# Optimization experiments

Hardware: AMD Instinct MI355X
Metric: run time of the kernel (lower is better)

The kernel has to match this reference:

```python
import jax, jax.numpy as jnp
import numpy as np

N, E, T = 10000, 160000, 1600000
D, C, H = 256, 64, 1024  # d_model, d_message/channels, 4*d_model ffn hidden


def setup_inputs() -> dict:
    key = jax.random.key(0)
    ks = jax.random.split(key, 20)
    rn = lambda k, s, sc=1.0: jax.random.normal(k, s, dtype=jnp.float32) * sc
    return {
        "x": rn(ks[0], (N, D)),
        "y": rn(ks[1], (E, D)),
        "r": rn(ks[2], (E, 3)),
        "src": jax.random.randint(ks[3], (E,), 0, N),
        "dst": jax.random.randint(ks[4], (E,), 0, N),
        "tsrc": jax.random.randint(ks[5], (T,), 0, E),
        "tdst": jax.random.randint(ks[6], (T,), 0, E),
        "W_src": rn(ks[7], (D, C), 0.05), "b_src": rn(ks[8], (C,), 0.05),
        "W_dst": rn(ks[9], (D, C), 0.05), "b_dst": rn(ks[10], (C,), 0.05),
        "W_edge": rn(ks[11], (D, C), 0.05), "b_edge": rn(ks[12], (C,), 0.05),
        "attn": rn(ks[13], (C,), 0.05),
        "W1": rn(ks[14], (C, H), 0.05), "b1": rn(ks[15], (H,), 0.05),
        "W2": rn(ks[16], (H, D), 0.05), "b2": rn(ks[17], (D,), 0.05),
    }


def reference(x, y, r, src, dst, tsrc, tdst,
              W_src, b_src, W_dst, b_dst, W_edge, b_edge,
              attn, W1, b1, W2, b2):
    # per-bond message: xij = Lin_src(x)[src] + Lin_dst(x)[dst] + Lin_edge(y)  -> (E, C)
    xij = (x @ W_src + b_src)[src] + (x @ W_dst + b_dst)[dst] + (y @ W_edge + b_edge)

    # triplet angle cosine via normalized (negated) bond vectors  -> (T,)
    rnorm = -r / jnp.linalg.norm(r, axis=1, keepdims=True)
    cos_jik = jnp.clip(jnp.sum(rnorm[tsrc] * rnorm[tdst], axis=-1), -1.0 + 1e-6, 1.0 - 1e-6)

    # Chebyshev expansion: T_n(cos) = cos(n * arccos(cos))  -> (T, C)
    n = jnp.arange(C, dtype=jnp.float32)
    z_jik = jnp.cos(n[None, :] * jnp.arccos(cos_jik)[:, None])

    # triplet feature and attention logit
    e_jik = jax.nn.silu(z_jik + xij[tsrc] + xij[tdst])          # (T, C)
    logits = e_jik @ attn                                        # (T,)

    # segment softmax over triplets grouped by destination bond (edge_softmax)
    mx = jax.ops.segment_max(logits, tdst, num_segments=E)
    ex = jnp.exp(logits - mx[tdst])
    den = jax.ops.segment_sum(ex, tdst, num_segments=E)
    a = ex / den[tdst]                                           # (T,)

    # attention-weighted scatter-sum of neighbor bond features  -> (E, C)
    ft = jax.ops.segment_sum(xij[tsrc] * a[:, None], tdst, num_segments=E)

    # feedforward: Linear -> SiLU -> Linear  -> (E, D)
    return jax.nn.silu(ft @ W1 + b1) @ W2 + b2
```

## Files before the change

kernel.cpp:

```cpp
#include <hip/hip_runtime.h>

#define N_NODES 10000
#define N_EDGES 160000
#define N_TRI   1600000
#define DM      256
#define CH      64
#define HH      1024

typedef short bf16x8 __attribute__((ext_vector_type(8)));
typedef float f32x4  __attribute__((ext_vector_type(4)));

__device__ __forceinline__ unsigned short f2bf(float f) {
  unsigned int u = __float_as_uint(f);
  u += 0x7fff + ((u >> 16) & 1);
  return (unsigned short)(u >> 16);
}

__global__ __launch_bounds__(256) void k_node_proj(
    const float* __restrict__ x, const float* __restrict__ Ws, const float* __restrict__ bs,
    const float* __restrict__ Wd, const float* __restrict__ bd,
    float* __restrict__ xs, float* __restrict__ xd) {
  __shared__ float xl[4][DM];
  int tid = threadIdx.x;
  int n0 = blockIdx.x * 4;
  for (int i = tid; i < 4 * DM; i += 256) xl[i >> 8][i & 255] = x[n0 * DM + i];
  __syncthreads();
  int c = tid & 63, g = tid >> 6;
  float as = bs[c], ad = bd[c];
  for (int d = 0; d < DM; d++) {
    float xv = xl[g][d];
    as += xv * Ws[d * CH + c];
    ad += xv * Wd[d * CH + c];
  }
  int n = n0 + g;
  xs[n * CH + c] = as;
  xd[n * CH + c] = ad;
}

__global__ __launch_bounds__(256) void k_edge_proj(
    const float* __restrict__ y, const float* __restrict__ We, const float* __restrict__ be,
    const float* __restrict__ xs, const float* __restrict__ xd,
    const int* __restrict__ src, const int* __restrict__ dst,
    float* __restrict__ xij) {
  __shared__ float yl[16][DM];
  int tid = threadIdx.x;
  int e0 = blockIdx.x * 16;
  for (int i = tid; i < 16 * DM; i += 256) yl[i >> 8][i & 255] = y[e0 * DM + i];
  __syncthreads();
  int c = tid & 63, g = tid >> 6;
  float acc[4];
#pragma unroll
  for (int s = 0; s < 4; s++) acc[s] = be[c];
  for (int d = 0; d < DM; d += 4) {
    float w0 = We[(d + 0) * CH + c];
    float w1 = We[(d + 1) * CH + c];
    float w2 = We[(d + 2) * CH + c];
    float w3 = We[(d + 3) * CH + c];
#pragma unroll
    for (int s = 0; s < 4; s++) {
      const float4 yv = *(const float4*)&yl[g * 4 + s][d];
      acc[s] += yv.x * w0 + yv.y * w1 + yv.z * w2 + yv.w * w3;
    }
  }
#pragma unroll
  for (int s = 0; s < 4; s++) {
    int e = e0 + g * 4 + s;
    xij[e * CH + c] = acc[s] + xs[src[e] * CH + c] + xd[dst[e] * CH + c];
  }
}

__global__ void k_rnorm(const float* __restrict__ r, float4* __restrict__ rn4) {
  int e = blockIdx.x * 256 + threadIdx.x;
  if (e >= N_EDGES) return;
  float a = r[e * 3 + 0], b = r[e * 3 + 1], c = r[e * 3 + 2];
  float inv = rsqrtf(a * a + b * b + c * c);
  rn4[e] = (float4){-a * inv, -b * inv, -c * inv, 0.f};
}

__global__ __launch_bounds__(256) void k_theta(
    const float4* __restrict__ rn4, const int* __restrict__ tsrc, const int* __restrict__ tdst,
    float* __restrict__ theta) {
  int t = blockIdx.x * 256 + threadIdx.x;
  if (t >= N_TRI) return;
  float4 a = rn4[tsrc[t]];
  float4 b = rn4[tdst[t]];
  float c = a.x * b.x + a.y * b.y + a.z * b.z;
  c = fminf(fmaxf(c, -1.0f + 1e-6f), 1.0f - 1e-6f);
  theta[t] = acosf(c);
}

__global__ void k_hist(const int* __restrict__ tdst, int* __restrict__ cnt) {
  int t = blockIdx.x * 256 + threadIdx.x;
  if (t < N_TRI) atomicAdd(&cnt[tdst[t]], 1);
}

__global__ __launch_bounds__(256) void k_scan_sum(const int* __restrict__ cnt,
                                                  int* __restrict__ bsum, int n) {
  __shared__ int s[256];
  int b = blockIdx.x, tid = threadIdx.x;
  int tot = 0;
#pragma unroll
  for (int i = 0; i < 8; i++) {
    int idx = b * 2048 + i * 256 + tid;
    if (idx < n) tot += cnt[idx];
  }
  s[tid] = tot;
  __syncthreads();
  for (int off = 128; off > 0; off >>= 1) {
    if (tid < off) s[tid] += s[tid + off];
    __syncthreads();
  }
  if (tid == 0) bsum[b] = s[0];
}

__global__ void k_scan_top(int* __restrict__ bsum, int nb, int* __restrict__ start_last) {
  if (threadIdx.x == 0) {
    int run = 0;
    for (int i = 0; i < nb; i++) {
      int v = bsum[i];
      bsum[i] = run;
      run += v;
    }
    *start_last = run;
  }
}

__global__ __launch_bounds__(256) void k_scan_apply(const int* __restrict__ cnt,
                                                    const int* __restrict__ bsum,
                                                    int* __restrict__ start,
                                                    int* __restrict__ cur, int n) {
  __shared__ int s[256];
  int b = blockIdx.x, tid = threadIdx.x;
  int base = b * 2048 + tid * 8;
  int loc[8];
  int tot = 0;
#pragma unroll
  for (int i = 0; i < 8; i++) {
    int idx = base + i;
    int v = (idx < n) ? cnt[idx] : 0;
    loc[i] = tot;
    tot += v;
  }
  s[tid] = tot;
  __syncthreads();
  for (int off = 1; off < 256; off <<= 1) {
    int t2 = 0;
    if (tid >= off) t2 = s[tid - off];
    __syncthreads();
    if (tid >= off) s[tid] += t2;
    __syncthreads();
  }
  int excl = s[tid] - tot + bsum[b];
#pragma unroll
  for (int i = 0; i < 8; i++) {
    int idx = base + i;
    if (idx < n) {
      int v = excl + loc[i];
      start[idx] = v;
      cur[idx] = v;
    }
  }
}

__global__ void k_scatter(const int* __restrict__ tdst, int* __restrict__ cur,
                          int* __restrict__ sorted) {
  int t = blockIdx.x * 256 + threadIdx.x;
  if (t < N_TRI) {
    int p = atomicAdd(&cur[tdst[t]], 1);
    sorted[p] = t;
  }
}

__global__ __launch_bounds__(256) void k_attn_ft(
    const int* __restrict__ start, const int* __restrict__ sorted,
    const float* __restrict__ theta, const int* __restrict__ tsrc,
    const float* __restrict__ xij, const float* __restrict__ attn,
    unsigned short* __restrict__ ft) {
  int tid = threadIdx.x;
  int e = blockIdx.x * 4 + (tid >> 6);
  int lane = tid & 63;
  float lanef = (float)lane;
  int beg = start[e], end = start[e + 1];
  int deg = end - beg;
  float xd = xij[e * CH + lane];
  float av = attn[lane];
  float m = -1e30f, den = 0.f, acc = 0.f;
  if (deg > 0 && deg <= 64) {
    int ts_ = 0;
    float th_ = 0.f;
    if (lane < deg) {
      int t = sorted[beg + lane];
      ts_ = tsrc[t];
      th_ = theta[t];
    }
    int ts_cur = __shfl(ts_, 0);
    float th_cur = __shfl(th_, 0);
    float xs_cur = xij[ts_cur * CH + lane];
    for (int i = 0; i < deg; i++) {
      float th_nxt = 0.f, xs_nxt = 0.f;
      if (i + 1 < deg) {
        int ts_nxt = __shfl(ts_, i + 1);
        th_nxt = __shfl(th_, i + 1);
        xs_nxt = xij[ts_nxt * CH + lane];
      }
      float v = __cosf(th_cur * lanef) + xs_cur + xd;
      float sv = v / (1.f + __expf(-v));
      float contrib = sv * av;
#pragma unroll
      for (int off = 32; off; off >>= 1) contrib += __shfl_xor(contrib, off);
      float mn = fmaxf(m, contrib);
      float scale = __expf(m - mn);
      float p = __expf(contrib - mn);
      den = den * scale + p;
      acc = acc * scale + p * xs_cur;
      m = mn;
      th_cur = th_nxt;
      xs_cur = xs_nxt;
    }
  } else if (deg > 64) {
    for (int i = 0; i < deg; i++) {
      int t = sorted[beg + i];
      int ts = tsrc[t];
      float th = theta[t];
      float xs = xij[ts * CH + lane];
      float v = __cosf(th * lanef) + xs + xd;
      float sv = v / (1.f + __expf(-v));
      float contrib = sv * av;
#pragma unroll
      for (int off = 32; off; off >>= 1) contrib += __shfl_xor(contrib, off);
      float mn = fmaxf(m, contrib);
      float scale = __expf(m - mn);
      float p = __expf(contrib - mn);
      den = den * scale + p;
      acc = acc * scale + p * xs;
      m = mn;
    }
  }
  ft[e * CH + lane] = f2bf(deg > 0 ? acc / den : 0.f);
}

__global__ __launch_bounds__(256) void k_prep_w1p(const float* __restrict__ W1,
                                                  unsigned short* __restrict__ W1P) {
  int idx = blockIdx.x * 256 + threadIdx.x;
  int k = idx & 63, row = idx >> 6;
  int i = row & 15, t = (row >> 4) & 1, hb = row >> 5;
  int hidden = hb * 32 + ((i >> 2) << 3) + (t << 2) + (i & 3);
  W1P[idx] = f2bf(W1[k * HH + hidden]);
}

__global__ __launch_bounds__(256) void k_prep_w2t(const float* __restrict__ W2,
                                                  unsigned short* __restrict__ W2T) {
  int idx = blockIdx.x * 256 + threadIdx.x;
  int n = idx >> 10, k = idx & 1023;
  W2T[idx] = f2bf(W2[k * DM + n]);
}

__global__ __launch_bounds__(256, 2) void k_ffn_mfma2(
    const unsigned short* __restrict__ ft, const unsigned short* __restrict__ W1P,
    const float* __restrict__ b1, const unsigned short* __restrict__ W2T,
    const float* __restrict__ b2, float* __restrict__ out) {
  int tid = threadIdx.x;
  int wave = tid >> 6, lane = tid & 63;
  int l16 = lane & 15, q = lane >> 4;
  int ebase = blockIdx.x * 128 + wave * 32;

  bf16x8 ftf[2][2];
#pragma unroll
  for (int mt = 0; mt < 2; mt++)
#pragma unroll
    for (int s = 0; s < 2; s++)
      ftf[mt][s] = *(const bf16x8*)&ft[(size_t)(ebase + mt * 16 + l16) * CH + s * 32 + q * 8];

  f32x4 acc[2][16];
#pragma unroll
  for (int mt = 0; mt < 2; mt++)
#pragma unroll
    for (int nt = 0; nt < 16; nt++) acc[mt][nt] = (f32x4){0.f, 0.f, 0.f, 0.f};

  bf16x8 w1f[2][2];
#pragma unroll
  for (int t = 0; t < 2; t++)
#pragma unroll
    for (int s = 0; s < 2; s++)
      w1f[t][s] = *(const bf16x8*)&W1P[(size_t)((t * 16) + l16) * 64 + s * 32 + q * 8];

  for (int hb = 0; hb < 32; hb++) {
    f32x4 h[2][2];
#pragma unroll
    for (int mt = 0; mt < 2; mt++)
#pragma unroll
      for (int t = 0; t < 2; t++) {
        f32x4 z = (f32x4){0.f, 0.f, 0.f, 0.f};
        z = __builtin_amdgcn_mfma_f32_16x16x32_bf16(w1f[t][0], ftf[mt][0], z, 0, 0, 0);
        z = __builtin_amdgcn_mfma_f32_16x16x32_bf16(w1f[t][1], ftf[mt][1], z, 0, 0, 0);
        h[mt][t] = z;
      }

    int hbn = (hb < 31) ? hb + 1 : 31;
    bf16x8 w1n[2][2];
#pragma unroll
    for (int t = 0; t < 2; t++)
#pragma unroll
      for (int s = 0; s < 2; s++)
        w1n[t][s] = *(const bf16x8*)&W1P[(size_t)((hbn * 2 + t) * 16 + l16) * 64 + s * 32 + q * 8];

    const float4 b1v0 = *(const float4*)&b1[hb * 32 + q * 8];
    const float4 b1v1 = *(const float4*)&b1[hb * 32 + q * 8 + 4];
    union { bf16x8 v; unsigned int u[4]; } pa[2];
#pragma unroll
    for (int mt = 0; mt < 2; mt++) {
      float v0 = h[mt][0][0] + b1v0.x, v1 = h[mt][0][1] + b1v0.y;
      float v2 = h[mt][0][2] + b1v0.z, v3 = h[mt][0][3] + b1v0.w;
      float w0 = h[mt][1][0] + b1v1.x, w1 = h[mt][1][1] + b1v1.y;
      float w2 = h[mt][1][2] + b1v1.z, w3 = h[mt][1][3] + b1v1.w;
      float s0 = v0 / (1.f + __expf(-v0)), s1 = v1 / (1.f + __expf(-v1));
      float s2 = v2 / (1.f + __expf(-v2)), s3 = v3 / (1.f + __expf(-v3));
      float t0 = w0 / (1.f + __expf(-w0)), t1 = w1 / (1.f + __expf(-w1));
      float t2 = w2 / (1.f + __expf(-w2)), t3 = w3 / (1.f + __expf(-w3));
      pa[mt].u[0] = ((unsigned int)f2bf(s1) << 16) | f2bf(s0);
      pa[mt].u[1] = ((unsigned int)f2bf(s3) << 16) | f2bf(s2);
      pa[mt].u[2] = ((unsigned int)f2bf(t1) << 16) | f2bf(t0);
      pa[mt].u[3] = ((unsigned int)f2bf(t3) << 16) | f2bf(t2);
    }

#pragma unroll
    for (int ng = 0; ng < 4; ng++) {
      bf16x8 bw[4];
#pragma unroll
      for (int i = 0; i < 4; i++)
        bw[i] = *(const bf16x8*)&W2T[(size_t)((ng * 4 + i) * 16 + l16) * HH + hb * 32 + q * 8];
#pragma unroll
      for (int i = 0; i < 4; i++) {
        acc[0][ng * 4 + i] =
            __builtin_amdgcn_mfma_f32_16x16x32_bf16(pa[0].v, bw[i], acc[0][ng * 4 + i], 0, 0, 0);
        acc[1][ng * 4 + i] =
            __builtin_amdgcn_mfma_f32_16x16x32_bf16(pa[1].v, bw[i], acc[1][ng * 4 + i], 0, 0, 0);
      }
    }

#pragma unroll
    for (int t = 0; t < 2; t++)
#pragma unroll
      for (int s = 0; s < 2; s++) w1f[t][s] = w1n[t][s];
  }

#pragma unroll
  for (int nt = 0; nt < 16; nt++) {
    float b2v = b2[nt * 16 + l16];
#pragma unroll
    for (int mt = 0; mt < 2; mt++) {
      int erow = ebase + mt * 16 + q * 4;
#pragma unroll
      for (int r = 0; r < 4; r++)
        out[(size_t)(erow + r) * DM + nt * 16 + l16] = acc[mt][nt][r] + b2v;
    }
  }
}

extern "C" void kernel_launch(void* const* d_in, const int* in_sizes, int n_in,
                              void* d_out, int out_size, void* d_ws, size_t ws_size,
                              hipStream_t stream) {
  (void)in_sizes; (void)n_in; (void)out_size; (void)ws_size;
  const float* x      = (const float*)d_in[0];
  const float* y      = (const float*)d_in[1];
  const float* r      = (const float*)d_in[2];
  const int*   src    = (const int*)d_in[3];
  const int*   dst    = (const int*)d_in[4];
  const int*   tsrc   = (const int*)d_in[5];
  const int*   tdst   = (const int*)d_in[6];
  const float* W_src  = (const float*)d_in[7];
  const float* b_src  = (const float*)d_in[8];
  const float* W_dst  = (const float*)d_in[9];
  const float* b_dst  = (const float*)d_in[10];
  const float* W_edge = (const float*)d_in[11];
  const float* b_edge = (const float*)d_in[12];
  const float* attn   = (const float*)d_in[13];
  const float* W1     = (const float*)d_in[14];
  const float* b1     = (const float*)d_in[15];
  const float* W2     = (const float*)d_in[16];
  const float* b2     = (const float*)d_in[17];
  float* out = (float*)d_out;

  char* wsp = (char*)d_ws;
  auto alloc = [&](size_t bytes) -> char* {
    char* p = wsp;
    wsp += (bytes + 255) & ~(size_t)255;
    return p;
  };
  float* xs     = (float*)alloc((size_t)N_NODES * CH * 4);
  float* xd     = (float*)alloc((size_t)N_NODES * CH * 4);
  float* xij    = (float*)alloc((size_t)N_EDGES * CH * 4);
  float4* rn4   = (float4*)alloc((size_t)N_EDGES * 16);
  float* theta  = (float*)alloc((size_t)N_TRI * 4);
  int*   cnt    = (int*)alloc((size_t)N_EDGES * 4);
  int*   start  = (int*)alloc((size_t)(N_EDGES + 1) * 4);
  int*   cur    = (int*)alloc((size_t)N_EDGES * 4);
  int*   bsum   = (int*)alloc(1024 * 4);
  int*   sorted = (int*)alloc((size_t)N_TRI * 4);
  unsigned short* ftb = (unsigned short*)alloc((size_t)N_EDGES * CH * 2);
  unsigned short* W1P = (unsigned short*)alloc((size_t)CH * HH * 2);
  unsigned short* W2T = (unsigned short*)alloc((size_t)HH * DM * 2);

  const int NB = (N_EDGES + 2047) / 2048;

  k_prep_w1p<<<(CH * HH) / 256, 256, 0, stream>>>(W1, W1P);
  k_prep_w2t<<<(HH * DM) / 256, 256, 0, stream>>>(W2, W2T);

  k_node_proj<<<N_NODES / 4, 256, 0, stream>>>(x, W_src, b_src, W_dst, b_dst, xs, xd);
  k_rnorm<<<N_EDGES / 256, 256, 0, stream>>>(r, rn4);
  k_edge_proj<<<N_EDGES / 16, 256, 0, stream>>>(y, W_edge, b_edge, xs, xd, src, dst, xij);
  k_theta<<<N_TRI / 256, 256, 0, stream>>>(rn4, tsrc, tdst, theta);

  hipMemsetAsync(cnt, 0, (size_t)N_EDGES * 4, stream);
  k_hist<<<N_TRI / 256, 256, 0, stream>>>(tdst, cnt);
  k_scan_sum<<<NB, 256, 0, stream>>>(cnt, bsum, N_EDGES);
  k_scan_top<<<1, 64, 0, stream>>>(bsum, NB, &start[N_EDGES]);
  k_scan_apply<<<NB, 256, 0, stream>>>(cnt, bsum, start, cur, N_EDGES);
  k_scatter<<<N_TRI / 256, 256, 0, stream>>>(tdst, cur, sorted);

  k_attn_ft<<<N_EDGES / 4, 256, 0, stream>>>(start, sorted, theta, tsrc, xij, attn, ftb);
  k_ffn_mfma2<<<N_EDGES / 128, 256, 0, stream>>>(ftb, W1P, b1, W2T, b2, out);
}
```

Measured before the change: 1.318 ms.

## Split FFN output columns across waves and share hidden activations via LDS

The FFN kernel now gives each block 64 edges, and each wave computes the hidden activations for its own 16 edges. Those activations go through a double-buffered shared-memory tile, so each wave can then produce a 64-column slice of the output for all 64 edges. This cuts accumulator registers from 32 to 16 tiles per wave and raises the occupancy target from 2 to 3 blocks. The costs are a __syncthreads per hidden block, extra LDS traffic, and twice as many blocks, each reading its own W2 slice.

```diff
diff --git a/kernel.cpp b/kernel.cpp
--- a/kernel.cpp
+++ b/kernel.cpp
@@ -255,46 +255,62 @@
   W2T[idx] = f2bf(W2[k * DM + n]);
 }
 
-__global__ __launch_bounds__(256, 2) void k_ffn_mfma2(
+__global__ __launch_bounds__(256, 3) void k_ffn_mfma3(
     const unsigned short* __restrict__ ft, const unsigned short* __restrict__ W1P,
     const float* __restrict__ b1, const unsigned short* __restrict__ W2T,
     const float* __restrict__ b2, float* __restrict__ out) {
+  __shared__ __align__(16) unsigned short hbuf[2][4 * 64 * 8];
   int tid = threadIdx.x;
-  int wave = tid >> 6, lane = tid & 63;
+  int w = tid >> 6, lane = tid & 63;
   int l16 = lane & 15, q = lane >> 4;
-  int ebase = blockIdx.x * 128 + wave * 32;
-
-  bf16x8 ftf[2][2];
-#pragma unroll
-  for (int mt = 0; mt < 2; mt++)
+  int e0 = blockIdx.x * 64;
+
+  bf16x8 ftf[2];
+#pragma unroll
+  for (int s = 0; s < 2; s++)
+    ftf[s] = *(const bf16x8*)&ft[(size_t)(e0 + w * 16 + l16) * CH + s * 32 + q * 8];
+
+  f32x4 acc[4][4];
+#pragma unroll
+  for (int mt = 0; mt < 4; mt++)
+#pragma unroll
+    for (int nt = 0; nt < 4; nt++) acc[mt][nt] = (f32x4){0.f, 0.f, 0.f, 0.f};
+
+  bf16x8 w1f[2][2];
+#pragma unroll
+  for (int t = 0; t < 2; t++)
 #pragma unroll
     for (int s = 0; s < 2; s++)
-      ftf[mt][s] = *(const bf16x8*)&ft[(size_t)(ebase + mt * 16 + l16) * CH + s * 32 + q * 8];
-
-  f32x4 acc[2][16];
-#pragma unroll
-  for (int mt = 0; mt < 2; mt++)
-#pragma unroll
-    for (int nt = 0; nt < 16; nt++) acc[mt][nt] = (f32x4){0.f, 0.f, 0.f, 0.f};
-
-  bf16x8 w1f[2][2];
-#pragma unroll
-  for (int t = 0; t < 2; t++)
-#pragma unroll
-    for (int s = 0; s < 2; s++)
-      w1f[t][s] = *(const bf16x8*)&W1P[(size_t)((t * 16) + l16) * 64 + s * 32 + q * 8];
-
+      w1f[t][s] = *(const bf16x8*)&W1P[(size_t)(t * 16 + l16) * 64 + s * 32 + q * 8];
+
+  int p = 0;
   for (int hb = 0; hb < 32; hb++) {
-    f32x4 h[2][2];
-#pragma unroll
-    for (int mt = 0; mt < 2; mt++)
-#pragma unroll
-      for (int t = 0; t < 2; t++) {
-        f32x4 z = (f32x4){0.f, 0.f, 0.f, 0.f};
-        z = __builtin_amdgcn_mfma_f32_16x16x32_bf16(w1f[t][0], ftf[mt][0], z, 0, 0, 0);
-        z = __builtin_amdgcn_mfma_f32_16x16x32_bf16(w1f[t][1], ftf[mt][1], z, 0, 0, 0);
-        h[mt][t] = z;
-      }
+    bf16x8 bw[4];
+#pragma unroll
+    for (int nt = 0; nt < 4; nt++)
+      bw[nt] = *(const bf16x8*)&W2T[(size_t)(w * 64 + nt * 16 + l16) * HH + hb * 32 + q * 8];
+
+    f32x4 h0 = (f32x4){0.f, 0.f, 0.f, 0.f};
+    f32x4 h1 = (f32x4){0.f, 0.f, 0.f, 0.f};
+    h0 = __builtin_amdgcn_mfma_f32_16x16x32_bf16(w1f[0][0], ftf[0], h0, 0, 0, 0);
+    h0 = __builtin_amdgcn_mfma_f32_16x16x32_bf16(w1f[0][1], ftf[1], h0, 0, 0, 0);
+    h1 = __builtin_amdgcn_mfma_f32_16x16x32_bf16(w1f[1][0], ftf[0], h1, 0, 0, 0);
+    h1 = __builtin_amdgcn_mfma_f32_16x16x32_bf16(w1f[1][1], ftf[1], h1, 0, 0, 0);
+
+    const float4 bv0 = *(const float4*)&b1[hb * 32 + q * 8];
+    const float4 bv1 = *(const float4*)&b1[hb * 32 + q * 8 + 4];
+    float v0 = h0[0] + bv0.x, v1 = h0[1] + bv0.y, v2 = h0[2] + bv0.z, v3 = h0[3] + bv0.w;
+    float w0 = h1[0] + bv1.x, w1_ = h1[1] + bv1.y, w2 = h1[2] + bv1.z, w3 = h1[3] + bv1.w;
+    float s0 = v0 / (1.f + __expf(-v0)), s1 = v1 / (1.f + __expf(-v1));
+    float s2 = v2 / (1.f + __expf(-v2)), s3 = v3 / (1.f + __expf(-v3));
+    float t0 = w0 / (1.f + __expf(-w0)), t1 = w1_ / (1.f + __expf(-w1_));
+    float t2 = w2 / (1.f + __expf(-w2)), t3 = w3 / (1.f + __expf(-w3));
+    union { bf16x8 v; unsigned int u[4]; } pa;
+    pa.u[0] = ((unsigned int)f2bf(s1) << 16) | f2bf(s0);
+    pa.u[1] = ((unsigned int)f2bf(s3) << 16) | f2bf(s2);
+    pa.u[2] = ((unsigned int)f2bf(t1) << 16) | f2bf(t0);
+    pa.u[3] = ((unsigned int)f2bf(t3) << 16) | f2bf(t2);
+    *(bf16x8*)&hbuf[p][(w * 64 + lane) * 8] = pa.v;
 
     int hbn = (hb < 31) ? hb + 1 : 31;
     bf16x8 w1n[2][2];
@@ -304,55 +320,35 @@
       for (int s = 0; s < 2; s++)
         w1n[t][s] = *(const bf16x8*)&W1P[(size_t)((hbn * 2 + t) * 16 + l16) * 64 + s * 32 + q * 8];
 
-    const float4 b1v0 = *(const float4*)&b1[hb * 32 + q * 8];
-    const float4 b1v1 = *(const float4*)&b1[hb * 32 + q * 8 + 4];
-    union { bf16x8 v; unsigned int u[4]; } pa[2];
-#pragma unroll
-    for (int mt = 0; mt < 2; mt++) {
-      float v0 = h[mt][0][0] + b1v0.x, v1 = h[mt][0][1] + b1v0.y;
-      float v2 = h[mt][0][2] + b1v0.z, v3 = h[mt][0][3] + b1v0.w;
-      float w0 = h[mt][1][0] + b1v1.x, w1 = h[mt][1][1] + b1v1.y;
-      float w2 = h[mt][1][2] + b1v1.z, w3 = h[mt][1][3] + b1v1.w;
-      float s0 = v0 / (1.f + __expf(-v0)), s1 = v1 / (1.f + __expf(-v1));
-      float s2 = v2 / (1.f + __expf(-v2)), s3 = v3 / (1.f + __expf(-v3));
-      float t0 = w0 / (1.f + __expf(-w0)), t1 = w1 / (1.f + __expf(-w1));
-      float t2 = w2 / (1.f + __expf(-w2)), t3 = w3 / (1.f + __expf(-w3));
-      pa[mt].u[0] = ((unsigned int)f2bf(s1) << 16) | f2bf(s0);
-      pa[mt].u[1] = ((unsigned int)f2bf(s3) << 16) | f2bf(s2);
-      pa[mt].u[2] = ((unsigned int)f2bf(t1) << 16) | f2bf(t0);
-      pa[mt].u[3] = ((unsigned int)f2bf(t3) << 16) | f2bf(t2);
-    }
-
-#pragma unroll
-    for (int ng = 0; ng < 4; ng++) {
-      bf16x8 bw[4];
-#pragma unroll
-      for (int i = 0; i < 4; i++)
-        bw[i] = *(const bf16x8*)&W2T[(size_t)((ng * 4 + i) * 16 + l16) * HH + hb * 32 + q * 8];
-#pragma unroll
-      for (int i = 0; i < 4; i++) {
-        acc[0][ng * 4 + i] =
-            __builtin_amdgcn_mfma_f32_16x16x32_bf16(pa[0].v, bw[i], acc[0][ng * 4 + i], 0, 0, 0);
-        acc[1][ng * 4 + i] =
-            __builtin_amdgcn_mfma_f32_16x16x32_bf16(pa[1].v, bw[i], acc[1][ng * 4 + i], 0, 0, 0);
-      }
-    }
+    __syncthreads();
+
+    bf16x8 pam[4];
+#pragma unroll
+    for (int mt = 0; mt < 4; mt++)
+      pam[mt] = *(const bf16x8*)&hbuf[p][(mt * 64 + lane) * 8];
+#pragma unroll
+    for (int nt = 0; nt < 4; nt++)
+#pragma unroll
+      for (int mt = 0; mt < 4; mt++)
+        acc[mt][nt] = __builtin_amdgcn_mfma_f32_16x16x32_bf16(pam[mt], bw[nt], acc[mt][nt], 0, 0, 0);
 
 #pragma unroll
     for (int t = 0; t < 2; t++)
 #pragma unroll
       for (int s = 0; s < 2; s++) w1f[t][s] = w1n[t][s];
-  }
-
-#pragma unroll
-  for (int nt = 0; nt < 16; nt++) {
-    float b2v = b2[nt * 16 + l16];
-#pragma unroll
-    for (int mt = 0; mt < 2; mt++) {
-      int erow = ebase + mt * 16 + q * 4;
+    p ^= 1;
+  }
+
+#pragma unroll
+  for (int nt = 0; nt < 4; nt++) {
+    int col = w * 64 + nt * 16 + l16;
+    float b2v = b2[col];
+#pragma unroll
+    for (int mt = 0; mt < 4; mt++) {
+      int erow = e0 + mt * 16 + q * 4;
 #pragma unroll
       for (int r = 0; r < 4; r++)
-        out[(size_t)(erow + r) * DM + nt * 16 + l16] = acc[mt][nt][r] + b2v;
+        out[(size_t)(erow + r) * DM + col] = acc[mt][nt][r] + b2v;
     }
   }
 }
@@ -419,5 +415,5 @@
   k_scatter<<<N_TRI / 256, 256, 0, stream>>>(tdst, cur, sorted);
 
   k_attn_ft<<<N_EDGES / 4, 256, 0, stream>>>(start, sorted, theta, tsrc, xij, attn, ftb);
-  k_ffn_mfma2<<<N_EDGES / 128, 256, 0, stream>>>(ftb, W1P, b1, W2T, b2, out);
-}
+  k_ffn_mfma3<<<N_EDGES / 64, 256, 0, stream>>>(ftb, W1P, b1, W2T, b2, out);
+}
```

Result: faster. 1.228 ms (-6.8%).
